# Kernel optimization log

Hardware: AMD Instinct MI355X
Metric: run time of the kernel (lower is better)

Reference implementation:

```python
import jax, jax.numpy as jnp
import numpy as np

B, C, H, N = 2, 128, 128, 2048   # batch, in_channels, hidden_dim, points per view
TEMP = 0.1
ITERS = 20
EPS = 1e-8


def setup_inputs() -> dict:
    key = jax.random.key(0)
    ks = jax.random.split(key, 4)
    s = lambda fan_in: 1.0 / np.sqrt(fan_in)
    return {
        "feat_d": jax.random.normal(ks[0], (B, C, N), jnp.float32),
        "feat_s": jax.random.normal(ks[1], (B, C, N), jnp.float32),
        # dustbin_head params: Conv1d(C->H, k=1) -> ReLU -> Conv1d(H->1, k=1)
        "W1": jax.random.normal(ks[2], (H, C), jnp.float32) * s(C),
        "b1": jnp.zeros((H,), jnp.float32),
        "W2": jax.random.normal(ks[3], (1, H), jnp.float32) * s(H),
        "b2": jnp.zeros((1,), jnp.float32),
    }


def _dustbin_head(x, W1, b1, W2, b2):
    # 1x1 Conv1d == channel matmul. x: [B, C, N] -> [B, 1, N]
    h = jax.nn.relu(jnp.einsum('hc,bcn->bhn', W1, x) + b1[None, :, None])
    return jnp.einsum('oh,bhn->bon', W2, h) + b2[None, :, None]


def _log_cross_view_ot(feat_q, feat_k, dustbin, temperature, iters):
    # scores: [B, Nq, Nk]; dustbin appended as the last row -> [B, Nq+1, Nk]
    scores = jnp.einsum('bcn,bcm->bnm', feat_q, feat_k) / temperature
    log_T0 = jnp.concatenate([scores, dustbin], axis=1)

    def step(log_T, _):
        log_T = log_T - jax.nn.logsumexp(log_T, axis=2, keepdims=True)  # row norm
        log_T = log_T - jax.nn.logsumexp(log_T, axis=1, keepdims=True)  # col norm
        return log_T, None

    log_T, _ = jax.lax.scan(step, log_T0, None, length=iters)
    return log_T


def reference(feat_d, feat_s, W1, b1, W2, b2):
    # N_d == N_s, so the torch F.interpolate calls are identity ops.
    dust_d = _dustbin_head(feat_d, W1, b1, W2, b2)  # [B, 1, N]
    dust_s = _dustbin_head(feat_s, W1, b1, W2, b2)  # [B, 1, N]

    log_T_ds = _log_cross_view_ot(feat_d, feat_s, dust_d, TEMP, ITERS)
    log_T_sd = _log_cross_view_ot(feat_s, feat_d, dust_s, TEMP, ITERS)

    T_ds = jnp.exp(log_T_ds[:, :-1, :])  # drop dustbin row -> [B, N, N]
    T_sd = jnp.exp(log_T_sd[:, :-1, :])

    loss_consistency = jnp.mean((T_ds - jnp.swapaxes(T_sd, 1, 2)) ** 2)

    entropy_ds = -(T_ds * jnp.log(T_ds + EPS)).sum(axis=(1, 2)).mean()
    entropy_sd = -(T_sd * jnp.log(T_sd + EPS)).sum(axis=(1, 2)).mean()
    loss_entropy = 0.5 * (entropy_ds + entropy_sd)

    return loss_consistency + 0.01 * loss_entropy
```

## Files before the change

### kernel.cpp

```cpp
#include <hip/hip_runtime.h>
#include <hip/hip_fp16.h>
#include <math.h>

#define NPTS 2048
#define NB 2
#define NC 128
#define NH 128
#define INV_TEMP 10.0f
#define NITERS 20
#define EPSF 1e-8f

static __device__ __forceinline__ void lse_merge(float& m, float& s, float m2, float s2){
  float M = fmaxf(m, m2);
  s = s * __expf(m - M) + s2 * __expf(m2 - M);
  m = M;
}

static __device__ __forceinline__ void unpack8(uint4 raw, float* x){
  float2 f;
  f = __half22float2(*(__half2*)&raw.x); x[0]=f.x; x[1]=f.y;
  f = __half22float2(*(((__half2*)&raw.x)+1)); x[2]=f.x; x[3]=f.y;
  f = __half22float2(*(__half2*)&raw.z); x[4]=f.x; x[5]=f.y;
  f = __half22float2(*(((__half2*)&raw.z)+1)); x[6]=f.x; x[7]=f.y;
}

static __device__ __forceinline__ float reduce32_lse(float* x){
  float mt[16];
  #pragma unroll
  for (int i = 0; i < 16; ++i) mt[i] = fmaxf(x[i], x[i + 16]);
  #pragma unroll
  for (int st = 8; st >= 1; st >>= 1)
    #pragma unroll
    for (int i = 0; i < 8; ++i) if (i < st) mt[i] = fmaxf(mt[i], mt[i + st]);
  float m = mt[0];
  float s0 = 0.f, s1 = 0.f, s2 = 0.f, s3 = 0.f;
  #pragma unroll
  for (int i = 0; i < 32; i += 4){
    s0 += __expf(x[i]     - m);
    s1 += __expf(x[i + 1] - m);
    s2 += __expf(x[i + 2] - m);
    s3 += __expf(x[i + 3] - m);
  }
  float s = (s0 + s1) + (s2 + s3);
  #pragma unroll
  for (int d = 1; d < 64; d <<= 1){
    float m2 = __shfl_xor(m, d);
    float sx = __shfl_xor(s, d);
    lse_merge(m, s, m2, sx);
  }
  return m + __logf(s);
}

__global__ __launch_bounds__(128) void dust_kernel(
    const float* __restrict__ fd, const float* __restrict__ fs,
    const float* __restrict__ W1, const float* __restrict__ b1,
    const float* __restrict__ W2, const float* __restrict__ b2,
    float* __restrict__ dust_d, float* __restrict__ dust_s){
  const int chunk = blockIdx.x, b = blockIdx.y, view = blockIdx.z;
  const float* x = (view == 0 ? fd : fs) + (size_t)b * NC * NPTS;
  float* out = (view == 0 ? dust_d : dust_s) + (size_t)b * NPTS;
  const int n0 = chunk * 16;
  __shared__ float xs[NC][17];
  __shared__ float red[NH][17];
  const int j = threadIdx.x;
  #pragma unroll
  for (int p = 0; p < 16; ++p) xs[j][p] = x[(size_t)j * NPTS + n0 + p];
  __syncthreads();
  float acc[16];
  float bb = b1[j];
  #pragma unroll
  for (int p = 0; p < 16; ++p) acc[p] = bb;
  for (int c = 0; c < NC; ++c){
    float w = W1[j * NC + c];
    #pragma unroll
    for (int p = 0; p < 16; ++p) acc[p] = fmaf(w, xs[c][p], acc[p]);
  }
  float w2 = W2[j];
  #pragma unroll
  for (int p = 0; p < 16; ++p) red[j][p] = w2 * fmaxf(acc[p], 0.0f);
  __syncthreads();
  for (int s = NH / 2; s >= 1; s >>= 1){
    if (j < s){
      #pragma unroll
      for (int p = 0; p < 16; ++p) red[j][p] += red[j + s][p];
    }
    __syncthreads();
  }
  if (j < 16) out[n0 + j] = red[0][j] + b2[0];
}

#define GP 68
#define KC 64
#define TP 68
__global__ __launch_bounds__(256) void gemm_kernel(
    const float* __restrict__ fd, const float* __restrict__ fs,
    __half* __restrict__ S, __half* __restrict__ ST){
  const int cb = blockIdx.x, rb = blockIdx.y, b = blockIdx.z;
  const float* A = fd + (size_t)b * NC * NPTS;
  const float* Bm = fs + (size_t)b * NC * NPTS;
  __shared__ float Als[KC * GP];
  __shared__ float Bls[KC * GP];
  const int tid = threadIdx.x;
  const int tx = tid & 15, ty = tid >> 4;
  float acc[4][4] = {};
  for (int kc = 0; kc < NC; kc += KC){
    for (int idx = tid; idx < KC * 64; idx += 256){
      int ch = idx >> 6, i = idx & 63;
      Als[ch * GP + i] = A[(size_t)(kc + ch) * NPTS + rb * 64 + i];
      Bls[ch * GP + i] = Bm[(size_t)(kc + ch) * NPTS + cb * 64 + i];
    }
    __syncthreads();
    for (int c = 0; c < KC; ++c){
      float4 a4 = *(const float4*)&Als[c * GP + ty * 4];
      float4 b4 = *(const float4*)&Bls[c * GP + tx * 4];
      float av[4] = {a4.x, a4.y, a4.z, a4.w};
      float bv[4] = {b4.x, b4.y, b4.z, b4.w};
      #pragma unroll
      for (int i = 0; i < 4; ++i)
        #pragma unroll
        for (int jj = 0; jj < 4; ++jj)
          acc[i][jj] = fmaf(av[i], bv[jj], acc[i][jj]);
    }
    __syncthreads();
  }
  __half* Sb = S + (size_t)b * NPTS * NPTS;
  __half* STb = ST + (size_t)b * NPTS * NPTS;
  const int r0 = rb * 64 + ty * 4, c0 = cb * 64 + tx * 4;
  #pragma unroll
  for (int i = 0; i < 4; ++i){
    __half2 p[2];
    p[0] = __float22half2_rn(make_float2(acc[i][0]*INV_TEMP, acc[i][1]*INV_TEMP));
    p[1] = __float22half2_rn(make_float2(acc[i][2]*INV_TEMP, acc[i][3]*INV_TEMP));
    *(uint2*)&Sb[(size_t)(r0 + i) * NPTS + c0] = *(uint2*)p;
  }
  __half* tl = (__half*)Als;
  #pragma unroll
  for (int i = 0; i < 4; ++i)
    #pragma unroll
    for (int jj = 0; jj < 4; ++jj)
      tl[(tx * 4 + jj) * TP + (ty * 4 + i)] = __float2half(acc[i][jj] * INV_TEMP);
  __syncthreads();
  #pragma unroll
  for (int i = 0; i < 4; ++i){
    const int cr = ty * 4 + i;
    *(uint2*)&STb[(size_t)(cb * 64 + cr) * NPTS + rb * 64 + tx * 4] =
        *(uint2*)&tl[cr * TP + tx * 4];
  }
}

__global__ __launch_bounds__(512, 4) void phase_kernel(
    const __half* __restrict__ S, const __half* __restrict__ ST,
    const float* __restrict__ dust_d, const float* __restrict__ dust_s,
    float* __restrict__ u_ds, float* __restrict__ u_sd,
    float* __restrict__ v_ds, float* __restrict__ v_sd,
    const int mode){
  const int b = blockIdx.y, mat = blockIdx.z;
  const int w = threadIdx.x >> 6, lane = threadIdx.x & 63;
  const int r = blockIdx.x * 8 + w;

  __shared__ float lds_off[NPTS];
  {
    const float* off;
    if (mode == 0) off = (mat == 0 ? v_ds : v_sd) + b * NPTS;
    else           off = (mat == 0 ? u_sd : u_ds) + b * (NPTS + 1);
    *(float4*)&lds_off[threadIdx.x * 4] = *(const float4*)&off[threadIdx.x * 4];
  }
  __syncthreads();

  {
    const __half* row = (mat == 0 ? S : ST) + ((size_t)b * NPTS + r) * NPTS;
    float x[32];
    #pragma unroll
    for (int k2 = 0; k2 < 4; ++k2){
      const int c = (k2 * 64 + lane) * 8;
      uint4 raw = *(const uint4*)&row[c];
      float xr[8];
      unpack8(raw, xr);
      float4 o0 = *(const float4*)&lds_off[c];
      float4 o1 = *(const float4*)&lds_off[c + 4];
      x[k2*8+0]=xr[0]+o0.x; x[k2*8+1]=xr[1]+o0.y; x[k2*8+2]=xr[2]+o0.z; x[k2*8+3]=xr[3]+o0.w;
      x[k2*8+4]=xr[4]+o1.x; x[k2*8+5]=xr[5]+o1.y; x[k2*8+6]=xr[6]+o1.z; x[k2*8+7]=xr[7]+o1.w;
    }
    float lse = reduce32_lse(x);
    if (lane == 0){
      if (mode == 0){
        (mat == 0 ? u_ds : u_sd)[b * (NPTS + 1) + r] = -lse;
      } else {
        float dsc = (mat == 0 ? dust_s : dust_d)[b * NPTS + r];
        float uN  = (mat == 0 ? u_sd : u_ds)[b * (NPTS + 1) + NPTS];
        float e = dsc + uN;
        float M2 = fmaxf(lse, e);
        lse = M2 + __logf(__expf(lse - M2) + __expf(e - M2));
        (mat == 0 ? v_sd : v_ds)[b * NPTS + r] = -lse;
      }
    }
  }

  if (mode == 0 && blockIdx.x == 0 && w == 0){
    const float* drow = (mat == 0 ? dust_d : dust_s) + b * NPTS;
    float x[32];
    #pragma unroll
    for (int k = 0; k < 8; ++k){
      const int c = (k * 64 + lane) * 4;
      float4 rv = *(const float4*)&drow[c];
      float4 o  = *(const float4*)&lds_off[c];
      x[k*4+0]=rv.x+o.x; x[k*4+1]=rv.y+o.y; x[k*4+2]=rv.z+o.z; x[k*4+3]=rv.w+o.w;
    }
    float lse = reduce32_lse(x);
    if (lane == 0)
      (mat == 0 ? u_ds : u_sd)[b * (NPTS + 1) + NPTS] = -lse;
  }
}

__global__ __launch_bounds__(512, 4) void loss_kernel(
    const __half* __restrict__ S,
    const float* __restrict__ u_ds, const float* __restrict__ u_sd,
    const float* __restrict__ v_ds, const float* __restrict__ v_sd,
    float* __restrict__ part){
  const int b = blockIdx.y;
  const int w = threadIdx.x >> 6, lane = threadIdx.x & 63;
  const int r = blockIdx.x * 8 + w;

  __shared__ float lds_vds[NPTS];
  __shared__ float lds_usd[NPTS];
  *(float4*)&lds_vds[threadIdx.x * 4] = *(const float4*)&v_ds[b * NPTS + threadIdx.x * 4];
  *(float4*)&lds_usd[threadIdx.x * 4] = *(const float4*)&u_sd[b * (NPTS + 1) + threadIdx.x * 4];
  __syncthreads();

  const __half* row = S + ((size_t)b * NPTS + r) * NPTS;
  const float uds = u_ds[b * (NPTS + 1) + r];
  const float vsd = v_sd[b * NPTS + r];
  float sd = 0.f, e1 = 0.f, e2 = 0.f;
  #pragma unroll
  for (int k2 = 0; k2 < 4; ++k2){
    const int c = (k2 * 64 + lane) * 8;
    uint4 raw = *(const uint4*)&row[c];
    float sv[8];
    unpack8(raw, sv);
    float4 a0 = *(const float4*)&lds_vds[c];
    float4 a1 = *(const float4*)&lds_vds[c + 4];
    float4 q0 = *(const float4*)&lds_usd[c];
    float4 q1 = *(const float4*)&lds_usd[c + 4];
    float av[8] = {a0.x,a0.y,a0.z,a0.w,a1.x,a1.y,a1.z,a1.w};
    float qv[8] = {q0.x,q0.y,q0.z,q0.w,q1.x,q1.y,q1.z,q1.w};
    #pragma unroll
    for (int i = 0; i < 8; ++i){
      float y1 = sv[i] + uds + av[i];
      float y2 = sv[i] + qv[i] + vsd;
      float t1 = __expf(y1);
      float t2 = __expf(y2);
      float d = t1 - t2;
      sd += d * d;
      e1 += t1 * y1;
      e2 += t2 * y2;
    }
  }
  #pragma unroll
  for (int d = 1; d < 64; d <<= 1){
    sd += __shfl_xor(sd, d);
    e1 += __shfl_xor(e1, d);
    e2 += __shfl_xor(e2, d);
  }
  if (lane == 0){
    float* p = part + ((size_t)b * NPTS + r) * 4;
    p[0] = sd; p[1] = e1; p[2] = e2;
  }
}

__global__ __launch_bounds__(256) void final_kernel(const float* __restrict__ part, float* __restrict__ out){
  const int tid = threadIdx.x;
  float s0 = 0.f, s1 = 0.f, s2 = 0.f;
  for (int i = tid; i < NB * NPTS; i += 256){
    s0 += part[(size_t)i * 4 + 0];
    s1 += part[(size_t)i * 4 + 1];
    s2 += part[(size_t)i * 4 + 2];
  }
  #pragma unroll
  for (int d = 1; d < 64; d <<= 1){
    s0 += __shfl_xor(s0, d);
    s1 += __shfl_xor(s1, d);
    s2 += __shfl_xor(s2, d);
  }
  __shared__ float rs[4][3];
  const int w = tid >> 6;
  if ((tid & 63) == 0){ rs[w][0] = s0; rs[w][1] = s1; rs[w][2] = s2; }
  __syncthreads();
  if (tid == 0){
    float a0 = rs[0][0] + rs[1][0] + rs[2][0] + rs[3][0];
    float a1 = rs[0][1] + rs[1][1] + rs[2][1] + rs[3][1];
    float a2 = rs[0][2] + rs[1][2] + rs[2][2] + rs[3][2];
    float lc = a0 / (float)((size_t)NB * NPTS * NPTS);
    float le = -0.5f * (a1 + a2) / (float)NB;
    out[0] = lc + 0.01f * le;
  }
}

extern "C" void kernel_launch(void* const* d_in, const int* in_sizes, int n_in,
                              void* d_out, int out_size, void* d_ws, size_t ws_size,
                              hipStream_t stream){
  const float* fd = (const float*)d_in[0];
  const float* fs = (const float*)d_in[1];
  const float* W1 = (const float*)d_in[2];
  const float* b1 = (const float*)d_in[3];
  const float* W2 = (const float*)d_in[4];
  const float* b2 = (const float*)d_in[5];
  char* ws = (char*)d_ws;
  __half* S  = (__half*)ws;
  __half* ST = S + (size_t)NB * NPTS * NPTS;
  float* fws = (float*)(ws + 2 * sizeof(__half) * (size_t)NB * NPTS * NPTS);
  float* dust_d = fws;
  float* dust_s = dust_d + (size_t)NB * NPTS;
  float* u_ds   = dust_s + (size_t)NB * NPTS;
  float* u_sd   = u_ds + (size_t)NB * (NPTS + 1);
  float* v_ds   = u_sd + (size_t)NB * (NPTS + 1);
  float* v_sd   = v_ds + (size_t)NB * NPTS;
  float* part   = v_sd + (size_t)NB * NPTS;

  hipMemsetAsync(v_ds, 0, sizeof(float) * (size_t)NB * NPTS * 2, stream);

  dust_kernel<<<dim3(NPTS / 16, NB, 2), 128, 0, stream>>>(fd, fs, W1, b1, W2, b2, dust_d, dust_s);
  gemm_kernel<<<dim3(NPTS / 64, NPTS / 64, NB), 256, 0, stream>>>(fd, fs, S, ST);
  const dim3 pgrid(NPTS / 8, NB, 2);
  for (int it = 0; it < NITERS; ++it){
    phase_kernel<<<pgrid, 512, 0, stream>>>(S, ST, dust_d, dust_s, u_ds, u_sd, v_ds, v_sd, 0);
    phase_kernel<<<pgrid, 512, 0, stream>>>(S, ST, dust_d, dust_s, u_ds, u_sd, v_ds, v_sd, 1);
  }
  loss_kernel<<<dim3(NPTS / 8, NB), 512, 0, stream>>>(S, u_ds, u_sd, v_ds, v_sd, part);
  final_kernel<<<1, 256, 0, stream>>>(part, (float*)d_out);
}
```

Baseline: 357.9 us.

## Fuse row and column Sinkhorn passes sharing the same matrix into one kernel

The Sinkhorn schedule is reordered so that each launch reads one matrix (S or ST) once and computes two reductions from it: the row-normalisation for one OT problem and the column-normalisation for the other. The original code read both S and ST on every phase. This roughly halves the matrix traffic per iteration, since the column update of one direction is the row pass over the shared transposed buffer. It adds a second LDS offset array and holds the raw row in registers, lowering the occupancy hint to 2. It also relies on the cross-direction dependency ordering being correct at the loop boundaries.

```diff
diff --git a/kernel.cpp b/kernel.cpp
--- a/kernel.cpp
+++ b/kernel.cpp
@@ -148,67 +148,78 @@
   }
 }
 
-__global__ __launch_bounds__(512, 4) void phase_kernel(
-    const __half* __restrict__ S, const __half* __restrict__ ST,
-    const float* __restrict__ dust_d, const float* __restrict__ dust_s,
-    float* __restrict__ u_ds, float* __restrict__ u_sd,
-    float* __restrict__ v_ds, float* __restrict__ v_sd,
-    const int mode){
-  const int b = blockIdx.y, mat = blockIdx.z;
+__global__ __launch_bounds__(512, 2) void phase2_kernel(
+    const __half* __restrict__ M,
+    const float* __restrict__ off1, const float* __restrict__ off2,
+    const float* __restrict__ dust1, const float* __restrict__ dust2,
+    float* __restrict__ out1, float* __restrict__ out2,
+    const int do_r1, const int do_r2)
+{
+  const int b = blockIdx.y;
   const int w = threadIdx.x >> 6, lane = threadIdx.x & 63;
   const int r = blockIdx.x * 8 + w;
 
-  __shared__ float lds_off[NPTS];
-  {
-    const float* off;
-    if (mode == 0) off = (mat == 0 ? v_ds : v_sd) + b * NPTS;
-    else           off = (mat == 0 ? u_sd : u_ds) + b * (NPTS + 1);
-    *(float4*)&lds_off[threadIdx.x * 4] = *(const float4*)&off[threadIdx.x * 4];
-  }
-  __syncthreads();
-
-  {
-    const __half* row = (mat == 0 ? S : ST) + ((size_t)b * NPTS + r) * NPTS;
+  __shared__ float lds_o1[NPTS];
+  __shared__ float lds_o2[NPTS];
+  *(float4*)&lds_o1[threadIdx.x * 4] = *(const float4*)&off1[b * NPTS + threadIdx.x * 4];
+  if (do_r2)
+    *(float4*)&lds_o2[threadIdx.x * 4] = *(const float4*)&off2[b * (NPTS + 1) + threadIdx.x * 4];
+  __syncthreads();
+
+  const __half* row = M + ((size_t)b * NPTS + r) * NPTS;
+  uint4 raw[4];
+  #pragma unroll
+  for (int k2 = 0; k2 < 4; ++k2) raw[k2] = *(const uint4*)&row[(k2 * 64 + lane) * 8];
+
+  if (do_r1){
     float x[32];
     #pragma unroll
     for (int k2 = 0; k2 < 4; ++k2){
       const int c = (k2 * 64 + lane) * 8;
-      uint4 raw = *(const uint4*)&row[c];
       float xr[8];
-      unpack8(raw, xr);
-      float4 o0 = *(const float4*)&lds_off[c];
-      float4 o1 = *(const float4*)&lds_off[c + 4];
+      unpack8(raw[k2], xr);
+      float4 o0 = *(const float4*)&lds_o1[c];
+      float4 o1 = *(const float4*)&lds_o1[c + 4];
       x[k2*8+0]=xr[0]+o0.x; x[k2*8+1]=xr[1]+o0.y; x[k2*8+2]=xr[2]+o0.z; x[k2*8+3]=xr[3]+o0.w;
       x[k2*8+4]=xr[4]+o1.x; x[k2*8+5]=xr[5]+o1.y; x[k2*8+6]=xr[6]+o1.z; x[k2*8+7]=xr[7]+o1.w;
     }
     float lse = reduce32_lse(x);
+    if (lane == 0) out1[b * (NPTS + 1) + r] = -lse;
+  }
+
+  if (do_r2){
+    float x[32];
+    #pragma unroll
+    for (int k2 = 0; k2 < 4; ++k2){
+      const int c = (k2 * 64 + lane) * 8;
+      float xr[8];
+      unpack8(raw[k2], xr);
+      float4 o0 = *(const float4*)&lds_o2[c];
+      float4 o1 = *(const float4*)&lds_o2[c + 4];
+      x[k2*8+0]=xr[0]+o0.x; x[k2*8+1]=xr[1]+o0.y; x[k2*8+2]=xr[2]+o0.z; x[k2*8+3]=xr[3]+o0.w;
+      x[k2*8+4]=xr[4]+o1.x; x[k2*8+5]=xr[5]+o1.y; x[k2*8+6]=xr[6]+o1.z; x[k2*8+7]=xr[7]+o1.w;
+    }
+    float lse = reduce32_lse(x);
     if (lane == 0){
-      if (mode == 0){
-        (mat == 0 ? u_ds : u_sd)[b * (NPTS + 1) + r] = -lse;
-      } else {
-        float dsc = (mat == 0 ? dust_s : dust_d)[b * NPTS + r];
-        float uN  = (mat == 0 ? u_sd : u_ds)[b * (NPTS + 1) + NPTS];
-        float e = dsc + uN;
-        float M2 = fmaxf(lse, e);
-        lse = M2 + __logf(__expf(lse - M2) + __expf(e - M2));
-        (mat == 0 ? v_sd : v_ds)[b * NPTS + r] = -lse;
-      }
-    }
-  }
-
-  if (mode == 0 && blockIdx.x == 0 && w == 0){
-    const float* drow = (mat == 0 ? dust_d : dust_s) + b * NPTS;
+      float e = dust2[b * NPTS + r] + off2[b * (NPTS + 1) + NPTS];
+      float M2 = fmaxf(lse, e);
+      lse = M2 + __logf(__expf(lse - M2) + __expf(e - M2));
+      out2[b * NPTS + r] = -lse;
+    }
+  }
+
+  if (do_r1 && blockIdx.x == 0 && w == 0){
+    const float* drow = dust1 + b * NPTS;
     float x[32];
     #pragma unroll
     for (int k = 0; k < 8; ++k){
       const int c = (k * 64 + lane) * 4;
       float4 rv = *(const float4*)&drow[c];
-      float4 o  = *(const float4*)&lds_off[c];
+      float4 o  = *(const float4*)&lds_o1[c];
       x[k*4+0]=rv.x+o.x; x[k*4+1]=rv.y+o.y; x[k*4+2]=rv.z+o.z; x[k*4+3]=rv.w+o.w;
     }
     float lse = reduce32_lse(x);
-    if (lane == 0)
-      (mat == 0 ? u_ds : u_sd)[b * (NPTS + 1) + NPTS] = -lse;
+    if (lane == 0) out1[b * (NPTS + 1) + NPTS] = -lse;
   }
 }
 
@@ -320,10 +331,13 @@
 
   dust_kernel<<<dim3(NPTS / 16, NB, 2), 128, 0, stream>>>(fd, fs, W1, b1, W2, b2, dust_d, dust_s);
   gemm_kernel<<<dim3(NPTS / 64, NPTS / 64, NB), 256, 0, stream>>>(fd, fs, S, ST);
-  const dim3 pgrid(NPTS / 8, NB, 2);
-  for (int it = 0; it < NITERS; ++it){
-    phase_kernel<<<pgrid, 512, 0, stream>>>(S, ST, dust_d, dust_s, u_ds, u_sd, v_ds, v_sd, 0);
-    phase_kernel<<<pgrid, 512, 0, stream>>>(S, ST, dust_d, dust_s, u_ds, u_sd, v_ds, v_sd, 1);
+
+  const dim3 pgrid(NPTS / 8, NB);
+  phase2_kernel<<<pgrid, 512, 0, stream>>>(S, v_ds, u_sd, dust_d, dust_s, u_ds, v_sd, 1, 0);
+  for (int k = 0; k < NITERS; ++k){
+    phase2_kernel<<<pgrid, 512, 0, stream>>>(ST, v_sd, u_ds, dust_s, dust_d, u_sd, v_ds, 1, 1);
+    phase2_kernel<<<pgrid, 512, 0, stream>>>(S, v_ds, u_sd, dust_d, dust_s, u_ds, v_sd,
+                                             (k + 1 < NITERS) ? 1 : 0, 1);
   }
   loss_kernel<<<dim3(NPTS / 8, NB), 512, 0, stream>>>(S, u_ds, u_sd, v_ds, v_sd, part);
   final_kernel<<<1, 256, 0, stream>>>(part, (float*)d_out);
```

Measured after the change: 372.2 us. 1.04x slower.
